# Kernel optimization log

Measured on AMD Instinct MI355X. Metric: run time of the kernel, lower is better.

The kernel has to match this reference:

```python
import jax, jax.numpy as jnp
import numpy as np

EPS = 1e-5

def _ln(x, g, b):
    m = jnp.mean(x, axis=-1, keepdims=True)
    v = jnp.mean((x - m) ** 2, axis=-1, keepdims=True)
    return (x - m) * jax.lax.rsqrt(v + EPS) * g + b


def setup_inputs() -> dict:
    key = jax.random.key(0)
    B, T, C, H, A = 4, 1024, 1024, 16, 64
    ks = jax.random.split(key, 16)
    s = 0.02
    inp = {
        "x": jax.random.normal(ks[0], (B, T, C), jnp.float32),
        "ln1_g": jnp.ones((C,), jnp.float32), "ln1_b": jnp.zeros((C,), jnp.float32),
        "ln2_g": jnp.ones((C,), jnp.float32), "ln2_b": jnp.zeros((C,), jnp.float32),
        "ln3_g": jnp.ones((C,), jnp.float32), "ln3_b": jnp.zeros((C,), jnp.float32),
        "wq": jax.random.normal(ks[1], (C, C), jnp.float32) * s, "bq": jnp.zeros((C,), jnp.float32),
        "wk": jax.random.normal(ks[2], (C, C), jnp.float32) * s, "bk": jnp.zeros((C,), jnp.float32),
        "wv": jax.random.normal(ks[3], (C, C), jnp.float32) * s, "bv": jnp.zeros((C,), jnp.float32),
        "wo": jax.random.normal(ks[4], (C, C), jnp.float32) * s, "bo": jnp.zeros((C,), jnp.float32),
        "w1": jax.random.normal(ks[5], (C, 4 * C), jnp.float32) * s, "b1": jnp.zeros((4 * C,), jnp.float32),
        "w2": jax.random.normal(ks[6], (4 * C, C), jnp.float32) * s, "b2": jnp.zeros((C,), jnp.float32),
        "wd": jax.random.normal(ks[7], (C, A), jnp.float32) * 1e-4, "bd": jnp.zeros((A,), jnp.float32),
        "wu": jax.random.normal(ks[8], (A, C), jnp.float32) * 1e-4, "bu": jnp.zeros((C,), jnp.float32),
    }
    return inp


def _block(x, ln1_g, ln1_b, ln2_g, ln2_b, ln3_g, ln3_b,
           wq, bq, wk, bk, wv, bv, wo, bo, w1, b1, w2, b2, wd, bd, wu, bu):
    B, T, C = x.shape
    H = 16
    D = C // H
    normed = _ln(x, ln3_g, ln3_b)  # ln3 of original input, used by adapter

    # --- causal self-attention on ln1(x) ---
    h = _ln(x, ln1_g, ln1_b)
    q = (h @ wq + bq).reshape(B, T, H, D)
    k = (h @ wk + bk).reshape(B, T, H, D)
    v = (h @ wv + bv).reshape(B, T, H, D)
    att = jnp.einsum('bqhd,bkhd->bhqk', q, k) * (1.0 / np.sqrt(D))
    causal = jnp.tril(jnp.ones((T, T), bool))
    att = jnp.where(causal, att, -jnp.inf)
    att = jax.nn.softmax(att, axis=-1)
    y = jnp.einsum('bhqk,bkhd->bqhd', att, v).reshape(B, T, C)
    attn_out = y @ wo + bo

    hidden = x + attn_out
    # --- MLP on ln2(hidden) ---
    m = _ln(hidden, ln2_g, ln2_b)
    mlp_out = jax.nn.gelu(m @ w1 + b1, approximate=False) @ w2 + b2
    forward_states = hidden + mlp_out

    # --- adapter on ln3(original x) ---
    a = jax.nn.relu(normed @ wd + bd) @ wu + bu

    # dropout is identity (p=0 / eval)
    return hidden + forward_states + a


def reference(x, ln1_g, ln1_b, ln2_g, ln2_b, ln3_g, ln3_b,
              wq, bq, wk, bk, wv, bv, wo, bo, w1, b1, w2, b2, wd, bd, wu, bu):
    return _block(x, ln1_g, ln1_b, ln2_g, ln2_b, ln3_g, ln3_b,
                  wq, bq, wk, bk, wv, bv, wo, bo, w1, b1, w2, b2, wd, bd, wu, bu)
```

## Files before the change

kernel.cpp:

```cpp
#include <hip/hip_runtime.h>

typedef unsigned short u16;
typedef __bf16 bf16x8 __attribute__((ext_vector_type(8)));
typedef u16    u16x8  __attribute__((ext_vector_type(8)));
typedef float  f32x4  __attribute__((ext_vector_type(4)));

__device__ __forceinline__ u16 f2bf(float f) {
    union { float f; unsigned u; } x{f};
    unsigned r = x.u + 0x7fffu + ((x.u >> 16) & 1u);
    return (u16)(r >> 16);
}

__device__ __forceinline__ f32x4 mfma16(bf16x8 a, bf16x8 b, f32x4 c) {
    return __builtin_amdgcn_mfma_f32_16x16x32_bf16(a, b, c, 0, 0, 0);
}

__device__ __forceinline__ void async_ld16(const void* g, void* l) {
    __builtin_amdgcn_global_load_lds(
        (const __attribute__((address_space(1))) unsigned int*)g,
        (__attribute__((address_space(3))) unsigned int*)l, 16, 0, 0);
}

__global__ void transpose_to_bf16(const float* __restrict__ in, u16* __restrict__ out,
                                  int K, int N) {
    __shared__ float tile[64][65];
    const int k0 = blockIdx.y * 64, n0 = blockIdx.x * 64;
    const int tid = threadIdx.x;
    const int rr = tid >> 4, cc = tid & 15;
#pragma unroll
    for (int it = 0; it < 4; ++it) {
        const int r = rr + it * 16;
        float4 v = *(const float4*)(in + (long)(k0 + r) * N + n0 + cc * 4);
        tile[r][cc * 4 + 0] = v.x; tile[r][cc * 4 + 1] = v.y;
        tile[r][cc * 4 + 2] = v.z; tile[r][cc * 4 + 3] = v.w;
    }
    __syncthreads();
#pragma unroll
    for (int it = 0; it < 4; ++it) {
        const int n = rr + it * 16;
        ushort4 o;
        o.x = f2bf(tile[cc * 4 + 0][n]);
        o.y = f2bf(tile[cc * 4 + 1][n]);
        o.z = f2bf(tile[cc * 4 + 2][n]);
        o.w = f2bf(tile[cc * 4 + 3][n]);
        *(ushort4*)(out + (long)(n0 + n) * K + k0 + cc * 4) = o;
    }
}

__global__ void concat_bias(const float* __restrict__ bq, const float* __restrict__ bk,
                            const float* __restrict__ bv, float* __restrict__ out) {
    int i = blockIdx.x * 256 + threadIdx.x;
    out[i] = i < 1024 ? bq[i] : (i < 2048 ? bk[i - 1024] : bv[i - 2048]);
}

__global__ void ln_dual_kernel(const float* __restrict__ x,
                               const float* __restrict__ g1, const float* __restrict__ b1,
                               const float* __restrict__ g3, const float* __restrict__ b3,
                               u16* __restrict__ out1, u16* __restrict__ out3) {
    const int row = blockIdx.x;
    const long base = (long)row * 1024;
    const int t = threadIdx.x;
    float4 v = ((const float4*)(x + base))[t];
    float s = v.x + v.y + v.z + v.w;
    float ss = v.x * v.x + v.y * v.y + v.z * v.z + v.w * v.w;
    for (int o = 32; o > 0; o >>= 1) { s += __shfl_down(s, o); ss += __shfl_down(ss, o); }
    __shared__ float red[8];
    if ((t & 63) == 0) { red[t >> 6] = s; red[(t >> 6) + 4] = ss; }
    __syncthreads();
    float sum = red[0] + red[1] + red[2] + red[3];
    float sq  = red[4] + red[5] + red[6] + red[7];
    const float mean = sum * (1.f / 1024.f);
    const float rstd = rsqrtf(sq * (1.f / 1024.f) - mean * mean + 1e-5f);
    float4 G1 = ((const float4*)g1)[t], B1 = ((const float4*)b1)[t];
    float4 G3 = ((const float4*)g3)[t], B3 = ((const float4*)b3)[t];
    float n0 = (v.x - mean) * rstd, n1 = (v.y - mean) * rstd;
    float n2 = (v.z - mean) * rstd, n3 = (v.w - mean) * rstd;
    ushort4 o1, o3;
    o1.x = f2bf(n0 * G1.x + B1.x); o1.y = f2bf(n1 * G1.y + B1.y);
    o1.z = f2bf(n2 * G1.z + B1.z); o1.w = f2bf(n3 * G1.w + B1.w);
    o3.x = f2bf(n0 * G3.x + B3.x); o3.y = f2bf(n1 * G3.y + B3.y);
    o3.z = f2bf(n2 * G3.z + B3.z); o3.w = f2bf(n3 * G3.w + B3.w);
    ((ushort4*)(out1 + base))[t] = o1;
    ((ushort4*)(out3 + base))[t] = o3;
}

__global__ void ln_single_kernel(const float* __restrict__ x,
                                 const float* __restrict__ g, const float* __restrict__ b,
                                 u16* __restrict__ out) {
    const int row = blockIdx.x;
    const long base = (long)row * 1024;
    const int t = threadIdx.x;
    float4 v = ((const float4*)(x + base))[t];
    float s = v.x + v.y + v.z + v.w;
    float ss = v.x * v.x + v.y * v.y + v.z * v.z + v.w * v.w;
    for (int o = 32; o > 0; o >>= 1) { s += __shfl_down(s, o); ss += __shfl_down(ss, o); }
    __shared__ float red[8];
    if ((t & 63) == 0) { red[t >> 6] = s; red[(t >> 6) + 4] = ss; }
    __syncthreads();
    float sum = red[0] + red[1] + red[2] + red[3];
    float sq  = red[4] + red[5] + red[6] + red[7];
    const float mean = sum * (1.f / 1024.f);
    const float rstd = rsqrtf(sq * (1.f / 1024.f) - mean * mean + 1e-5f);
    float4 G = ((const float4*)g)[t], B = ((const float4*)b)[t];
    ushort4 o;
    o.x = f2bf((v.x - mean) * rstd * G.x + B.x);
    o.y = f2bf((v.y - mean) * rstd * G.y + B.y);
    o.z = f2bf((v.z - mean) * rstd * G.z + B.z);
    o.w = f2bf((v.w - mean) * rstd * G.w + B.w);
    ((ushort4*)(out + base))[t] = o;
}

__global__ void transpose_v(const u16* __restrict__ qkv, u16* __restrict__ vT) {
    const int bh = blockIdx.z, b = bh >> 4, hh = bh & 15;
    const int t0 = blockIdx.x * 32, d0 = blockIdx.y * 32;
    __shared__ u16 tile[32][33];
    const u16* src = qkv + (long)(b * 1024) * 3072 + 2048 + hh * 64;
    for (int i = threadIdx.y; i < 32; i += 8)
        tile[i][threadIdx.x] = src[(long)(t0 + i) * 3072 + d0 + threadIdx.x];
    __syncthreads();
    u16* dst = vT + (long)bh * 64 * 1024;
    for (int i = threadIdx.y; i < 32; i += 8)
        dst[(long)(d0 + i) * 1024 + t0 + threadIdx.x] = tile[threadIdx.x][i];
}

template <typename Epi>
__global__ __launch_bounds__(256, 3)
void gemm_kernel(const u16* __restrict__ A, const u16* __restrict__ Bt,
                 int M, int N, int K, Epi epi) {
    __shared__ u16 smA[128 * 32];
    __shared__ u16 smB[128 * 32];
    const int tid = threadIdx.x;
    const int m0 = blockIdx.y * 128;
    const int n0 = blockIdx.x * 128;
    const int wid = tid >> 6, lane = tid & 63;
    const int wm = (wid >> 1) * 64, wn = (wid & 1) * 64;
    const int lr = lane & 15, lh = lane >> 4;

    const int cr = lane >> 2;
    const int lq = lane & 3;
    const int r0 = wid * 32 + cr;
    const int r1 = wid * 32 + 16 + cr;
    const int q0 = lq ^ (r0 & 3) ^ ((r0 >> 2) & 3);
    const int q1 = lq ^ (r1 & 3) ^ ((r1 >> 2) & 3);
    const int br0 = min(n0 + r0, N - 1);
    const int br1 = min(n0 + r1, N - 1);
    const long aoff0 = (long)(m0 + r0) * K + q0 * 8;
    const long aoff1 = (long)(m0 + r1) * K + q1 * 8;
    const long boff0 = (long)br0 * K + q0 * 8;
    const long boff1 = (long)br1 * K + q1 * 8;
    u16* ldsA0 = smA + (wid * 2    ) * 512;
    u16* ldsA1 = smA + (wid * 2 + 1) * 512;
    u16* ldsB0 = smB + (wid * 2    ) * 512;
    u16* ldsB1 = smB + (wid * 2 + 1) * 512;

    const int rs = (lr & 3) ^ ((lr >> 2) & 3);
    const int qoff = ((lh ^ rs) & 3) * 8;

    f32x4 acc[4][4] = {};

    const int nk = K / 32;
    for (int kt = 0; kt < nk; ++kt) {
        const long ko = (long)kt * 32;
        __syncthreads();
        async_ld16(A + aoff0 + ko, ldsA0);
        async_ld16(A + aoff1 + ko, ldsA1);
        async_ld16(Bt + boff0 + ko, ldsB0);
        async_ld16(Bt + boff1 + ko, ldsB1);
        __syncthreads();

        bf16x8 af[4], bfr[4];
#pragma unroll
        for (int i = 0; i < 4; ++i)
            af[i] = *(const bf16x8*)(smA + (wm + i * 16 + lr) * 32 + qoff);
#pragma unroll
        for (int j = 0; j < 4; ++j)
            bfr[j] = *(const bf16x8*)(smB + (wn + j * 16 + lr) * 32 + qoff);
#pragma unroll
        for (int i = 0; i < 4; ++i)
#pragma unroll
            for (int j = 0; j < 4; ++j)
                acc[i][j] = mfma16(af[i], bfr[j], acc[i][j]);
    }

#pragma unroll
    for (int i = 0; i < 4; ++i)
#pragma unroll
        for (int j = 0; j < 4; ++j) {
            const int col = n0 + wn + j * 16 + lr;
            if (col < N) {
#pragma unroll
                for (int r = 0; r < 4; ++r) {
                    const int row = m0 + wm + i * 16 + lh * 4 + r;
                    epi(row, col, acc[i][j][r]);
                }
            }
        }
}

struct EpiBF16Bias {
    u16* out; const float* bias; int ldo;
    __device__ void operator()(int r, int c, float v) const {
        out[(long)r * ldo + c] = f2bf(v + bias[c]);
    }
};
struct EpiResid {
    float* hidden; const float* bias; const float* x;
    __device__ void operator()(int r, int c, float v) const {
        long i = (long)r * 1024 + c; hidden[i] = v + bias[c] + x[i];
    }
};
struct EpiGelu {
    u16* out; const float* bias;
    __device__ void operator()(int r, int c, float v) const {
        float x = v + bias[c];
        float g = 0.5f * x * (1.f + erff(x * 0.70710678118654752f));
        out[(long)r * 4096 + c] = f2bf(g);
    }
};
struct EpiReluBF16 {
    u16* out; const float* bias;
    __device__ void operator()(int r, int c, float v) const {
        out[(long)r * 64 + c] = f2bf(fmaxf(v + bias[c], 0.f));
    }
};
struct EpiAdapter {
    float* out; const float* bias; const float* hidden;
    __device__ void operator()(int r, int c, float v) const {
        long i = (long)r * 1024 + c; out[i] = 2.f * hidden[i] + v + bias[c];
    }
};
struct EpiAddOut {
    float* out; const float* bias;
    __device__ void operator()(int r, int c, float v) const {
        long i = (long)r * 1024 + c; out[i] += v + bias[c];
    }
};

__global__ __launch_bounds__(256, 2)
void attn_kernel(const u16* __restrict__ qkv, const u16* __restrict__ vT,
                 u16* __restrict__ y) {
    const int bh = blockIdx.x, b = bh >> 4, hh = bh & 15;
    const int q0 = blockIdx.y * 128;
    const int tid = threadIdx.x, wid = tid >> 6, lane = tid & 63;
    const int lr = lane & 15, lh = lane >> 4;
    const int qw = q0 + wid * 32;

    __shared__ u16 smK[64 * 72];
    __shared__ u16 smV[64 * 72];
    __shared__ u16 smP[4 * 32 * 72];
    u16* pw = smP + wid * (32 * 72);

    const u16* qbase = qkv + (long)(b * 1024) * 3072 + hh * 64;
    const u16* kbase = qbase + 1024;
    const u16* vbase = vT + (long)bh * 64 * 1024;

    bf16x8 a_q[2][2];
#pragma unroll
    for (int mt = 0; mt < 2; ++mt)
#pragma unroll
        for (int ks = 0; ks < 2; ++ks) {
            uint4 t = *(const uint4*)(qbase + (long)(qw + mt * 16 + lr) * 3072 + ks * 32 + lh * 8);
            a_q[mt][ks] = __builtin_bit_cast(bf16x8, t);
        }

    bf16x8 ones;
    { u16x8 t = {0x3F80, 0x3F80, 0x3F80, 0x3F80, 0x3F80, 0x3F80, 0x3F80, 0x3F80};
      ones = __builtin_bit_cast(bf16x8, t); }

    f32x4 o_acc[2][4] = {};
    f32x4 l_acc[2] = {};
    f32x4 m_run[2] = {{-1e30f, -1e30f, -1e30f, -1e30f}, {-1e30f, -1e30f, -1e30f, -1e30f}};

    const int ntiles = q0 / 64 + 2;
    const int ck = tid >> 3, cs = (tid & 7) * 8;
    const int ck2 = (tid + 256) >> 3, cs2 = ((tid + 256) & 7) * 8;
    for (int kt = 0; kt < ntiles; ++kt) {
        const int k0 = kt * 64;
        __syncthreads();
        {
            uint4 kv0 = *(const uint4*)(kbase + (long)(k0 + ck) * 3072 + cs);
            uint4 kv1 = *(const uint4*)(kbase + (long)(k0 + ck2) * 3072 + cs2);
            *(uint4*)(smK + ck * 72 + cs) = kv0;
            *(uint4*)(smK + ck2 * 72 + cs2) = kv1;
            uint4 vv0 = *(const uint4*)(vbase + (long)ck * 1024 + k0 + cs);
            uint4 vv1 = *(const uint4*)(vbase + (long)ck2 * 1024 + k0 + cs2);
            *(uint4*)(smV + ck * 72 + cs) = vv0;
            *(uint4*)(smV + ck2 * 72 + cs2) = vv1;
        }
        __syncthreads();
        if (k0 > qw + 31) continue;

        bf16x8 bK[4][2];
#pragma unroll
        for (int nt = 0; nt < 4; ++nt)
#pragma unroll
            for (int ks = 0; ks < 2; ++ks)
                bK[nt][ks] = *(const bf16x8*)(smK + (nt * 16 + lr) * 72 + ks * 32 + lh * 8);

        f32x4 s[2][4];
#pragma unroll
        for (int mt = 0; mt < 2; ++mt)
#pragma unroll
            for (int nt = 0; nt < 4; ++nt) {
                f32x4 z = {0.f, 0.f, 0.f, 0.f};
                z = mfma16(a_q[mt][0], bK[nt][0], z);
                z = mfma16(a_q[mt][1], bK[nt][1], z);
                s[mt][nt] = z;
            }
#pragma unroll
        for (int mt = 0; mt < 2; ++mt) {
            const int qb = qw + mt * 16 + lh * 4;
#pragma unroll
            for (int nt = 0; nt < 4; ++nt) {
                const int kkg = k0 + nt * 16 + lr;
#pragma unroll
                for (int r = 0; r < 4; ++r) {
                    float v = s[mt][nt][r] * 0.125f;
                    if (kkg > qb + r) v = -1e30f;
                    s[mt][nt][r] = v;
                }
            }
        }
#pragma unroll
        for (int mt = 0; mt < 2; ++mt) {
            f32x4 mx = s[mt][0];
#pragma unroll
            for (int nt = 1; nt < 4; ++nt)
#pragma unroll
                for (int r = 0; r < 4; ++r) mx[r] = fmaxf(mx[r], s[mt][nt][r]);
#pragma unroll
            for (int xm = 1; xm < 16; xm <<= 1)
#pragma unroll
                for (int r = 0; r < 4; ++r) mx[r] = fmaxf(mx[r], __shfl_xor(mx[r], xm));
            f32x4 mnew, alpha;
#pragma unroll
            for (int r = 0; r < 4; ++r) {
                mnew[r] = fmaxf(m_run[mt][r], mx[r]);
                alpha[r] = __expf(m_run[mt][r] - mnew[r]);
            }
            m_run[mt] = mnew;
            l_acc[mt] *= alpha;
#pragma unroll
            for (int dt = 0; dt < 4; ++dt) o_acc[mt][dt] *= alpha;
#pragma unroll
            for (int nt = 0; nt < 4; ++nt)
#pragma unroll
                for (int r = 0; r < 4; ++r)
                    s[mt][nt][r] = __expf(s[mt][nt][r] - mnew[r]);
#pragma unroll
            for (int nt = 0; nt < 4; ++nt)
#pragma unroll
                for (int r = 0; r < 4; ++r)
                    pw[(mt * 16 + lh * 4 + r) * 72 + nt * 16 + lr] = f2bf(s[mt][nt][r]);
        }
        bf16x8 vf[4][2];
#pragma unroll
        for (int dt = 0; dt < 4; ++dt)
#pragma unroll
            for (int ks = 0; ks < 2; ++ks)
                vf[dt][ks] = *(const bf16x8*)(smV + (dt * 16 + lr) * 72 + ks * 32 + lh * 8);
#pragma unroll
        for (int mt = 0; mt < 2; ++mt) {
            bf16x8 pf0 = *(const bf16x8*)(pw + (mt * 16 + lr) * 72 + lh * 8);
            bf16x8 pf1 = *(const bf16x8*)(pw + (mt * 16 + lr) * 72 + 32 + lh * 8);
            l_acc[mt] = mfma16(pf0, ones, l_acc[mt]);
            l_acc[mt] = mfma16(pf1, ones, l_acc[mt]);
#pragma unroll
            for (int dt = 0; dt < 4; ++dt) {
                o_acc[mt][dt] = mfma16(pf0, vf[dt][0], o_acc[mt][dt]);
                o_acc[mt][dt] = mfma16(pf1, vf[dt][1], o_acc[mt][dt]);
            }
        }
    }
#pragma unroll
    for (int mt = 0; mt < 2; ++mt) {
        f32x4 linv;
#pragma unroll
        for (int r = 0; r < 4; ++r) linv[r] = 1.f / l_acc[mt][r];
#pragma unroll
        for (int dt = 0; dt < 4; ++dt) {
#pragma unroll
            for (int r = 0; r < 4; ++r) {
                const int tok = b * 1024 + qw + mt * 16 + lh * 4 + r;
                y[(long)tok * 1024 + hh * 64 + dt * 16 + lr] = f2bf(o_acc[mt][dt][r] * linv[r]);
            }
        }
    }
}

extern "C" void kernel_launch(void* const* d_in, const int* in_sizes, int n_in,
                              void* d_out, int out_size, void* d_ws, size_t ws_size,
                              hipStream_t stream) {
    const float* x    = (const float*)d_in[0];
    const float* ln1g = (const float*)d_in[1];
    const float* ln1b = (const float*)d_in[2];
    const float* ln2g = (const float*)d_in[3];
    const float* ln2b = (const float*)d_in[4];
    const float* ln3g = (const float*)d_in[5];
    const float* ln3b = (const float*)d_in[6];
    const float* wq = (const float*)d_in[7];  const float* bq = (const float*)d_in[8];
    const float* wk = (const float*)d_in[9];  const float* bk = (const float*)d_in[10];
    const float* wv = (const float*)d_in[11]; const float* bv = (const float*)d_in[12];
    const float* wo = (const float*)d_in[13]; const float* bo = (const float*)d_in[14];
    const float* w1 = (const float*)d_in[15]; const float* b1 = (const float*)d_in[16];
    const float* w2 = (const float*)d_in[17]; const float* b2 = (const float*)d_in[18];
    const float* wd = (const float*)d_in[19]; const float* bd = (const float*)d_in[20];
    const float* wu = (const float*)d_in[21]; const float* bu = (const float*)d_in[22];
    float* out = (float*)d_out;

    char* base = (char*)d_ws;
    size_t off = 0;
    auto carve = [&](size_t bytes) -> char* {
        char* p = base + off; off += (bytes + 255) & ~(size_t)255; return p;
    };
    u16* qkv_wt = (u16*)carve(3072L * 1024 * 2);
    u16* wo_t   = (u16*)carve(1024L * 1024 * 2);
    u16* w1_t   = (u16*)carve(4096L * 1024 * 2);
    u16* w2_t   = (u16*)carve(1024L * 4096 * 2);
    u16* wd_t   = (u16*)carve(64L * 1024 * 2);
    u16* wu_t   = (u16*)carve(1024L * 64 * 2);
    float* bqkv = (float*)carve(3072L * 4);
    u16* hbuf   = (u16*)carve(4096L * 1024 * 2);
    u16* nrm    = (u16*)carve(4096L * 1024 * 2);
    u16* qkvb   = (u16*)carve(4096L * 3072 * 2);
    u16* vT     = (u16*)carve(64L * 64 * 1024 * 2);
    u16* ybuf   = (u16*)carve(4096L * 1024 * 2);
    float* hid  = (float*)carve(4096L * 1024 * 4);
    u16* mbuf   = (u16*)carve(4096L * 1024 * 2);
    u16* act    = (u16*)carve(4096L * 4096 * 2);
    u16* t1     = (u16*)carve(4096L * 64 * 2);

    transpose_to_bf16<<<dim3(16, 16), 256, 0, stream>>>(wq, qkv_wt, 1024, 1024);
    transpose_to_bf16<<<dim3(16, 16), 256, 0, stream>>>(wk, qkv_wt + 1024L * 1024, 1024, 1024);
    transpose_to_bf16<<<dim3(16, 16), 256, 0, stream>>>(wv, qkv_wt + 2048L * 1024, 1024, 1024);
    transpose_to_bf16<<<dim3(16, 16), 256, 0, stream>>>(wo, wo_t, 1024, 1024);
    transpose_to_bf16<<<dim3(64, 16), 256, 0, stream>>>(w1, w1_t, 1024, 4096);
    transpose_to_bf16<<<dim3(16, 64), 256, 0, stream>>>(w2, w2_t, 4096, 1024);
    transpose_to_bf16<<<dim3(1, 16), 256, 0, stream>>>(wd, wd_t, 1024, 64);
    transpose_to_bf16<<<dim3(16, 1), 256, 0, stream>>>(wu, wu_t, 64, 1024);
    concat_bias<<<12, 256, 0, stream>>>(bq, bk, bv, bqkv);

    ln_dual_kernel<<<4096, 256, 0, stream>>>(x, ln1g, ln1b, ln3g, ln3b, hbuf, nrm);

    gemm_kernel<<<dim3(24, 32), 256, 0, stream>>>(hbuf, qkv_wt, 4096, 3072, 1024,
                                                  EpiBF16Bias{qkvb, bqkv, 3072});
    transpose_v<<<dim3(32, 2, 64), dim3(32, 8), 0, stream>>>(qkvb, vT);
    attn_kernel<<<dim3(64, 8), 256, 0, stream>>>(qkvb, vT, ybuf);
    gemm_kernel<<<dim3(8, 32), 256, 0, stream>>>(ybuf, wo_t, 4096, 1024, 1024,
                                                 EpiResid{hid, bo, x});
    ln_single_kernel<<<4096, 256, 0, stream>>>(hid, ln2g, ln2b, mbuf);
    gemm_kernel<<<dim3(32, 32), 256, 0, stream>>>(mbuf, w1_t, 4096, 4096, 1024,
                                                  EpiGelu{act, b1});
    gemm_kernel<<<dim3(1, 32), 256, 0, stream>>>(nrm, wd_t, 4096, 64, 1024,
                                                 EpiReluBF16{t1, bd});
    gemm_kernel<<<dim3(8, 32), 256, 0, stream>>>(t1, wu_t, 4096, 1024, 64,
                                                 EpiAdapter{out, bu, hid});
    gemm_kernel<<<dim3(8, 32), 256, 0, stream>>>(act, w2_t, 4096, 1024, 4096,
                                                 EpiAddOut{out, b2});
}
```

Baseline: 488.4 us.

## Multi-buffer GEMM LDS with async prefetch and add 128x64 tile variant

The GEMM kernel now uses a four-slot LDS ring buffer. It prefetches the next two K-tiles with async global-to-LDS loads while computing the current two, so it syncs once per two tiles instead of twice per tile. A BN=64 template variant is added and used for the N=1024 and N=64 GEMMs to raise block count and improve CU fill. Launch bounds drop to 2 blocks per SM because LDS use grows. There is a risk that the prefetched slots are overwritten before all waves finish reading them, since stage(kt+2) writes slot (kt+2)&3, which was last read in the previous iteration, after that iteration's barrier.

```diff
diff --git a/kernel.cpp b/kernel.cpp
--- a/kernel.cpp
+++ b/kernel.cpp
@@ -123,67 +123,86 @@
         dst[(long)(d0 + i) * 1024 + t0 + threadIdx.x] = tile[threadIdx.x][i];
 }
 
-template <typename Epi>
-__global__ __launch_bounds__(256, 3)
+template <int BN, typename Epi>
+__global__ __launch_bounds__(256, 2)
 void gemm_kernel(const u16* __restrict__ A, const u16* __restrict__ Bt,
                  int M, int N, int K, Epi epi) {
-    __shared__ u16 smA[128 * 32];
-    __shared__ u16 smB[128 * 32];
+    constexpr int AE = 128 * 32;
+    constexpr int BE = BN * 32;
+    constexpr int MI = (BN == 128) ? 4 : 2;
+    __shared__ u16 sm[4][AE + BE];
     const int tid = threadIdx.x;
     const int m0 = blockIdx.y * 128;
-    const int n0 = blockIdx.x * 128;
+    const int n0 = blockIdx.x * BN;
     const int wid = tid >> 6, lane = tid & 63;
-    const int wm = (wid >> 1) * 64, wn = (wid & 1) * 64;
     const int lr = lane & 15, lh = lane >> 4;
-
-    const int cr = lane >> 2;
-    const int lq = lane & 3;
-    const int r0 = wid * 32 + cr;
-    const int r1 = wid * 32 + 16 + cr;
-    const int q0 = lq ^ (r0 & 3) ^ ((r0 >> 2) & 3);
-    const int q1 = lq ^ (r1 & 3) ^ ((r1 >> 2) & 3);
-    const int br0 = min(n0 + r0, N - 1);
-    const int br1 = min(n0 + r1, N - 1);
-    const long aoff0 = (long)(m0 + r0) * K + q0 * 8;
-    const long aoff1 = (long)(m0 + r1) * K + q1 * 8;
-    const long boff0 = (long)br0 * K + q0 * 8;
-    const long boff1 = (long)br1 * K + q1 * 8;
-    u16* ldsA0 = smA + (wid * 2    ) * 512;
-    u16* ldsA1 = smA + (wid * 2 + 1) * 512;
-    u16* ldsB0 = smB + (wid * 2    ) * 512;
-    u16* ldsB1 = smB + (wid * 2 + 1) * 512;
-
-    const int rs = (lr & 3) ^ ((lr >> 2) & 3);
-    const int qoff = ((lh ^ rs) & 3) * 8;
-
-    f32x4 acc[4][4] = {};
-
+    const int wm = (BN == 128) ? (wid >> 1) * 64 : wid * 32;
+    const int wn = (BN == 128) ? (wid & 1) * 64 : 0;
+
+    const int cr = lane >> 2, lq = lane & 3;
+    const int ra0 = wid * 32 + cr, ra1 = ra0 + 16;
+    const int qa0 = lq ^ (ra0 & 3) ^ ((ra0 >> 2) & 3);
+    const int qa1 = lq ^ (ra1 & 3) ^ ((ra1 >> 2) & 3);
+    const long aoff0 = (long)(m0 + ra0) * K + qa0 * 8;
+    const long aoff1 = (long)(m0 + ra1) * K + qa1 * 8;
+    const int la0 = wid * 1024, la1 = la0 + 512;
+
+    long boff0, boff1 = 0;
+    int lb0, lb1 = 0;
+    if (BN == 128) {
+        boff0 = (long)min(n0 + ra0, N - 1) * K + qa0 * 8;
+        boff1 = (long)min(n0 + ra1, N - 1) * K + qa1 * 8;
+        lb0 = AE + wid * 1024; lb1 = lb0 + 512;
+    } else {
+        const int rb = wid * 16 + cr;
+        const int qb = lq ^ (rb & 3) ^ ((rb >> 2) & 3);
+        boff0 = (long)min(n0 + rb, N - 1) * K + qb * 8;
+        lb0 = AE + wid * 512;
+    }
+
+    const int qoff = ((lh ^ (lr & 3) ^ ((lr >> 2) & 3)) & 3) * 8;
+
+    f32x4 acc[MI][4] = {};
     const int nk = K / 32;
-    for (int kt = 0; kt < nk; ++kt) {
+
+    auto stage = [&](int kt) {
         const long ko = (long)kt * 32;
-        __syncthreads();
-        async_ld16(A + aoff0 + ko, ldsA0);
-        async_ld16(A + aoff1 + ko, ldsA1);
-        async_ld16(Bt + boff0 + ko, ldsB0);
-        async_ld16(Bt + boff1 + ko, ldsB1);
-        __syncthreads();
-
-        bf16x8 af[4], bfr[4];
-#pragma unroll
-        for (int i = 0; i < 4; ++i)
-            af[i] = *(const bf16x8*)(smA + (wm + i * 16 + lr) * 32 + qoff);
+        u16* s = sm[kt & 3];
+        async_ld16(A + aoff0 + ko, s + la0);
+        async_ld16(A + aoff1 + ko, s + la1);
+        async_ld16(Bt + boff0 + ko, s + lb0);
+        if constexpr (BN == 128) async_ld16(Bt + boff1 + ko, s + lb1);
+    };
+    auto compute = [&](int kt) {
+        const u16* sA = sm[kt & 3];
+        const u16* sB = sA + AE;
+        bf16x8 af[MI], bfr[4];
+#pragma unroll
+        for (int i = 0; i < MI; ++i)
+            af[i] = *(const bf16x8*)(sA + (wm + i * 16 + lr) * 32 + qoff);
 #pragma unroll
         for (int j = 0; j < 4; ++j)
-            bfr[j] = *(const bf16x8*)(smB + (wn + j * 16 + lr) * 32 + qoff);
-#pragma unroll
-        for (int i = 0; i < 4; ++i)
+            bfr[j] = *(const bf16x8*)(sB + (wn + j * 16 + lr) * 32 + qoff);
+#pragma unroll
+        for (int i = 0; i < MI; ++i)
 #pragma unroll
             for (int j = 0; j < 4; ++j)
                 acc[i][j] = mfma16(af[i], bfr[j], acc[i][j]);
-    }
-
-#pragma unroll
-    for (int i = 0; i < 4; ++i)
+    };
+
+    stage(0);
+    stage(1);
+    __syncthreads();
+    for (int kt = 0; kt < nk; kt += 2) {
+        if (kt + 2 < nk) stage(kt + 2);
+        if (kt + 3 < nk) stage(kt + 3);
+        compute(kt);
+        compute(kt + 1);
+        __syncthreads();
+    }
+
+#pragma unroll
+    for (int i = 0; i < MI; ++i)
 #pragma unroll
         for (int j = 0; j < 4; ++j) {
             const int col = n0 + wn + j * 16 + lr;
@@ -442,19 +461,19 @@
 
     ln_dual_kernel<<<4096, 256, 0, stream>>>(x, ln1g, ln1b, ln3g, ln3b, hbuf, nrm);
 
-    gemm_kernel<<<dim3(24, 32), 256, 0, stream>>>(hbuf, qkv_wt, 4096, 3072, 1024,
-                                                  EpiBF16Bias{qkvb, bqkv, 3072});
+    gemm_kernel<128><<<dim3(24, 32), 256, 0, stream>>>(hbuf, qkv_wt, 4096, 3072, 1024,
+                                                       EpiBF16Bias{qkvb, bqkv, 3072});
     transpose_v<<<dim3(32, 2, 64), dim3(32, 8), 0, stream>>>(qkvb, vT);
     attn_kernel<<<dim3(64, 8), 256, 0, stream>>>(qkvb, vT, ybuf);
-    gemm_kernel<<<dim3(8, 32), 256, 0, stream>>>(ybuf, wo_t, 4096, 1024, 1024,
-                                                 EpiResid{hid, bo, x});
+    gemm_kernel<64><<<dim3(16, 32), 256, 0, stream>>>(ybuf, wo_t, 4096, 1024, 1024,
+                                                      EpiResid{hid, bo, x});
     ln_single_kernel<<<4096, 256, 0, stream>>>(hid, ln2g, ln2b, mbuf);
-    gemm_kernel<<<dim3(32, 32), 256, 0, stream>>>(mbuf, w1_t, 4096, 4096, 1024,
-                                                  EpiGelu{act, b1});
-    gemm_kernel<<<dim3(1, 32), 256, 0, stream>>>(nrm, wd_t, 4096, 64, 1024,
-                                                 EpiReluBF16{t1, bd});
-    gemm_kernel<<<dim3(8, 32), 256, 0, stream>>>(t1, wu_t, 4096, 1024, 64,
-                                                 EpiAdapter{out, bu, hid});
-    gemm_kernel<<<dim3(8, 32), 256, 0, stream>>>(act, w2_t, 4096, 1024, 4096,
-                                                 EpiAddOut{out, b2});
-}
+    gemm_kernel<128><<<dim3(32, 32), 256, 0, stream>>>(mbuf, w1_t, 4096, 4096, 1024,
+                                                       EpiGelu{act, b1});
+    gemm_kernel<64><<<dim3(1, 32), 256, 0, stream>>>(nrm, wd_t, 4096, 64, 1024,
+                                                     EpiReluBF16{t1, bd});
+    gemm_kernel<64><<<dim3(16, 32), 256, 0, stream>>>(t1, wu_t, 4096, 1024, 64,
+                                                      EpiAdapter{out, bu, hid});
+    gemm_kernel<128><<<dim3(8, 32), 256, 0, stream>>>(act, w2_t, 4096, 1024, 4096,
+                                                      EpiAddOut{out, b2});
+}
```

Result: faster. 430.0 us (-11.9%).
